# Kernel optimization log

Measured on AMD Instinct MI355X. Metric: run time of the kernel, lower is better.

Reference implementation:

```python
import jax, jax.numpy as jnp
import numpy as np

N, K, F, NRBF = 10000, 32, 128, 300
GAMMA = 10.0


def ssp(x):
    # shifted softplus: softplus(x) - log(2)
    return jax.nn.softplus(x) - jnp.log(2.0).astype(x.dtype)


def setup_inputs() -> dict:
    key = jax.random.key(0)
    ks = jax.random.split(key, 12)
    s = lambda fan_in: 1.0 / np.sqrt(fan_in)
    inp = {
        "xyz": jax.random.normal(ks[0], (N, 3), jnp.float32) * 5.0,
        "atomic": jax.random.normal(ks[1], (N, F), jnp.float32),
        "edge_mask": (jax.random.uniform(ks[2], (N, K)) < 0.9).astype(jnp.float32),
        "src": jax.random.randint(ks[3], (N, K), 0, N),
        # pre_conv Linear(F, F) with bias
        "W_pre": jax.random.uniform(ks[4], (F, F), jnp.float32, -s(F), s(F)),
        "b_pre": jax.random.uniform(ks[5], (F,), jnp.float32, -s(F), s(F)),
        # cfconv: Linear(300, F, bias=False), SSP, Linear(F, F, bias=False), SSP
        "W_cf1": jax.random.uniform(ks[6], (NRBF, F), jnp.float32, -s(NRBF), s(NRBF)),
        "W_cf2": jax.random.uniform(ks[7], (F, F), jnp.float32, -s(F), s(F)),
        # post_conv: Linear(F,F), SSP, Linear(F,F)
        "W_post1": jax.random.uniform(ks[8], (F, F), jnp.float32, -s(F), s(F)),
        "b_post1": jax.random.uniform(ks[9], (F,), jnp.float32, -s(F), s(F)),
        "W_post2": jax.random.uniform(ks[10], (F, F), jnp.float32, -s(F), s(F)),
        "b_post2": jax.random.uniform(ks[11], (F,), jnp.float32, -s(F), s(F)),
        "rbf_centers": jnp.linspace(0.1, 30.1, NRBF, dtype=jnp.float32),
    }
    return inp


def reference(xyz, atomic, edge_mask, src, W_pre, b_pre, W_cf1, W_cf2,
              W_post1, b_post1, W_post2, b_post2, rbf_centers):
    pre = atomic @ W_pre + b_pre                       # [N, F]
    nbr_xyz = xyz[src]                                 # gather: [N, K, 3]
    d_ij = jnp.linalg.norm(nbr_xyz - xyz[:, None, :], axis=2, keepdims=True)  # [N, K, 1]
    rbf = jnp.exp(-GAMMA * (d_ij - rbf_centers[None, None, :]) ** 2)          # [N, K, 300]
    filters = ssp(ssp(rbf @ W_cf1) @ W_cf2)            # [N, K, F]
    conv_out = jnp.sum(filters * pre[src] * edge_mask[:, :, None], axis=1)    # [N, F]
    post = ssp(conv_out @ W_post1 + b_post1) @ W_post2 + b_post2
    return atomic + post
```

## Files before the change

### kernel.cpp

```cpp
#include <hip/hip_runtime.h>

#define NATOMS 10000
#define KNB 32
#define FD 128
#define NRBF 300
#define STEPC (30.0f / 299.0f)
#define INVSTEP (299.0f / 30.0f)
#define TROWS 256

typedef short short8 __attribute__((ext_vector_type(8)));
typedef float f32x4 __attribute__((ext_vector_type(4)));
typedef unsigned int u32x4 __attribute__((ext_vector_type(4)));

__device__ __forceinline__ unsigned short f2bf_rne(float f) {
    unsigned int u = __float_as_uint(f);
    u = (u + 0x7fffu + ((u >> 16) & 1u)) >> 16;
    return (unsigned short)u;
}

__device__ __forceinline__ unsigned int pack_bf2(float hi, float lo) {
    return __builtin_amdgcn_perm(__float_as_uint(hi) + 0x8000u,
                                 __float_as_uint(lo) + 0x8000u, 0x07060302u);
}

__device__ __forceinline__ unsigned short f2bf_rhu(float f) {
    return (unsigned short)((__float_as_uint(f) + 0x8000u) >> 16);
}

__device__ __forceinline__ float ssp_fast(float x) {
    float t = __builtin_amdgcn_exp2f(x * 1.44269504f);
    float l = __builtin_amdgcn_logf(1.0f + t);
    return 0.69314718056f * (l - 1.0f);
}

__device__ __forceinline__ float ssp_poly(float x) {
    float u = x * x;
    float p = fmaf(u, 2.1356923e-6f, -2.6351976e-5f);
    p = fmaf(u, p, 3.2552083e-4f);
    p = fmaf(u, p, -5.2083333e-3f);
    p = fmaf(u, p, 0.125f);
    return fmaf(0.5f, x, u * p);
}

__device__ __forceinline__ void gload_lds16(const void* g, void* l) {
    __builtin_amdgcn_global_load_lds(
        (const __attribute__((address_space(1))) unsigned int*)g,
        (__attribute__((address_space(3))) unsigned int*)l, 16, 0, 0);
}

__device__ __forceinline__ short8 rbf_row8(float d, float cg) {
    float t = d - cg;
    t = fminf(3.5f, fmaxf(-3.5f, t));
    float r = __builtin_amdgcn_exp2f(-14.4269504f * t * t);
    float q = __builtin_amdgcn_exp2f((28.8539008f * STEPC) * t
                                     - (14.4269504f * STEPC * STEPC));
    const float QRATIO = 0.81763172f;
    u32x4 p;
#pragma unroll
    for (int jj = 0; jj < 4; ++jj) {
        float v0 = r; r *= q; q *= QRATIO;
        float v1 = r; r *= q; q *= QRATIO;
        p[jj] = pack_bf2(v1, v0);
    }
    return __builtin_bit_cast(short8, p);
}

__global__ __launch_bounds__(256) void prep_pack(
    const float* __restrict__ Wcf1, const float* __restrict__ Wpre,
    const float* __restrict__ Wcf2, const float* __restrict__ Wpost1,
    const float* __restrict__ Wpost2, unsigned short* __restrict__ w1p,
    unsigned short* __restrict__ w4p) {
    int idx = blockIdx.x * 256 + threadIdx.x;
    if (idx < 40960) {
        int j = idx & 7, c = (idx >> 3) & 127, g = (idx >> 10) & 3, kc = idx >> 12;
        int k = kc * 32 + g * 8 + j;
        float v = (k < NRBF) ? Wcf1[k * FD + c] : 0.f;
        w1p[idx] = f2bf_rne(v);
    } else if (idx < 40960 + 65536) {
        int t = idx - 40960;
        int sel = t >> 14;
        int t2 = t & 16383;
        int j = t2 & 7, c = (t2 >> 3) & 127, g = (t2 >> 10) & 3, kc = t2 >> 12;
        int k = kc * 32 + g * 8 + j;
        const float* W = (sel == 0) ? Wpre : (sel == 1) ? Wcf2 : (sel == 2) ? Wpost1 : Wpost2;
        w4p[t] = f2bf_rne(W[k * FD + c]);
    }
}

__global__ __launch_bounds__(256) void pre_and_table(
    const float* __restrict__ X, const unsigned short* __restrict__ Wp,
    const float* __restrict__ bias, unsigned int* __restrict__ preP,
    const unsigned short* __restrict__ w1p, const unsigned short* __restrict__ w2p,
    unsigned int* __restrict__ T) {
    __shared__ unsigned short A2[128][132];
    const int tid = threadIdx.x;
    const int w = tid >> 6, lane = tid & 63, g = lane >> 4, c16 = lane & 15;

    if (blockIdx.x < 157) {
        const int r0 = blockIdx.x * 64 + w * 16;
        f32x4 acc[8];
#pragma unroll
        for (int b = 0; b < 8; ++b) acc[b] = (f32x4){0.f, 0.f, 0.f, 0.f};
        int row = r0 + c16;
        if (row >= NATOMS) row = 0;
#pragma unroll
        for (int kc = 0; kc < 4; ++kc) {
            const float* p0 = X + (size_t)row * FD + kc * 32 + g * 8;
            float4 xa = *(const float4*)p0, xb = *(const float4*)(p0 + 4);
            u32x4 pa;
            pa[0] = pack_bf2(xa.y, xa.x); pa[1] = pack_bf2(xa.w, xa.z);
            pa[2] = pack_bf2(xb.y, xb.x); pa[3] = pack_bf2(xb.w, xb.z);
            short8 a0 = __builtin_bit_cast(short8, pa);
            const unsigned short* wb = Wp + (kc * 4 + g) * 1024 + c16 * 8;
#pragma unroll
            for (int nb = 0; nb < 8; ++nb) {
                short8 b = *(const short8*)(wb + nb * 128);
                acc[nb] = __builtin_amdgcn_mfma_f32_16x16x32_bf16(a0, b, acc[nb], 0, 0, 0);
            }
        }
        float bv[8];
#pragma unroll
        for (int nb = 0; nb < 8; ++nb) bv[nb] = bias[nb * 16 + c16];
#pragma unroll
        for (int q = 0; q < 4; ++q) {
            int orow = r0 + 4 * g + q;
            if (orow < NATOMS) {
#pragma unroll
                for (int p2 = 0; p2 < 4; ++p2) {
                    float v0 = acc[2 * p2][q] + bv[2 * p2];
                    float v1 = acc[2 * p2 + 1][q] + bv[2 * p2 + 1];
                    preP[orow * 64 + c16 * 4 + p2] = pack_bf2(v1, v0);
                }
            }
        }
        return;
    }

    const int rbase = (int)(blockIdx.x - 157) * 128 + w * 32;
    const float hstep = 0.125f;
    const float d0 = (float)(rbase + c16) * hstep;
    const float d1 = (float)(rbase + 16 + c16) * hstep;

    const float BAND = 1.05f;
    float lo = (float)rbase * hstep, hi = (float)(rbase + 31) * hstep;
    int L = max(0, (int)floorf(((lo - BAND - 0.1f) * INVSTEP - 31.f) * 0.03125f));
    int H = min(9, (int)floorf(((hi + BAND - 0.1f) * INVSTEP) * 0.03125f));

    f32x4 acc[2][8];
#pragma unroll
    for (int a = 0; a < 2; ++a)
#pragma unroll
        for (int b = 0; b < 8; ++b) acc[a][b] = (f32x4){0.f, 0.f, 0.f, 0.f};

    for (int kc = L; kc <= H; ++kc) {
        const unsigned short* wb = w1p + kc * 4096 + g * 1024 + c16 * 8;
        short8 bfr[8];
#pragma unroll
        for (int nb = 0; nb < 8; ++nb) bfr[nb] = *(const short8*)(wb + nb * 128);
        const float cg = 0.1f + (float)(kc * 32 + g * 8) * STEPC;
        short8 a0 = rbf_row8(d0, cg);
        short8 a1 = rbf_row8(d1, cg);
#pragma unroll
        for (int nb = 0; nb < 8; ++nb) {
            acc[0][nb] = __builtin_amdgcn_mfma_f32_16x16x32_bf16(a0, bfr[nb], acc[0][nb], 0, 0, 0);
            acc[1][nb] = __builtin_amdgcn_mfma_f32_16x16x32_bf16(a1, bfr[nb], acc[1][nb], 0, 0, 0);
        }
    }

#pragma unroll
    for (int mr = 0; mr < 2; ++mr)
#pragma unroll
        for (int nb = 0; nb < 8; ++nb)
#pragma unroll
            for (int q = 0; q < 4; ++q) {
                int row = w * 32 + mr * 16 + 4 * g + q;
                A2[row][nb * 16 + c16] = f2bf_rhu(ssp_poly(acc[mr][nb][q]));
            }

    f32x4 acc2[2][8];
#pragma unroll
    for (int a = 0; a < 2; ++a)
#pragma unroll
        for (int b = 0; b < 8; ++b) acc2[a][b] = (f32x4){0.f, 0.f, 0.f, 0.f};

#pragma unroll
    for (int kc = 0; kc < 4; ++kc) {
        short8 a0 = *(const short8*)&A2[w * 32 + c16][kc * 32 + g * 8];
        short8 a1 = *(const short8*)&A2[w * 32 + 16 + c16][kc * 32 + g * 8];
        const unsigned short* wb = w2p + (kc * 4 + g) * 1024 + c16 * 8;
#pragma unroll
        for (int nb = 0; nb < 8; ++nb) {
            short8 b = *(const short8*)(wb + nb * 128);
            acc2[0][nb] = __builtin_amdgcn_mfma_f32_16x16x32_bf16(a0, b, acc2[0][nb], 0, 0, 0);
            acc2[1][nb] = __builtin_amdgcn_mfma_f32_16x16x32_bf16(a1, b, acc2[1][nb], 0, 0, 0);
        }
    }

#pragma unroll
    for (int mr = 0; mr < 2; ++mr)
#pragma unroll
        for (int q = 0; q < 4; ++q) {
            int r = rbase + mr * 16 + 4 * g + q;
#pragma unroll
            for (int p2 = 0; p2 < 4; ++p2) {
                float F0 = ssp_poly(acc2[mr][2 * p2][q]);
                float F1 = ssp_poly(acc2[mr][2 * p2 + 1][q]);
                T[r * 64 + c16 * 4 + p2] =
                    ((unsigned int)f2bf_rne(F1) << 16) | f2bf_rne(F0);
            }
        }
}

__global__ __launch_bounds__(512, 4) void conv_post(
    const float* __restrict__ xyz, const int* __restrict__ src,
    const float* __restrict__ mask, const unsigned int* __restrict__ preP,
    const unsigned int* __restrict__ T, const unsigned short* __restrict__ w1,
    const float* __restrict__ b1, const unsigned short* __restrict__ w2,
    const float* __restrict__ b2, const float* __restrict__ resid,
    float* __restrict__ Y) {
    __shared__ unsigned int Tl[TROWS * 64];
    __shared__ unsigned short Aconv[16][132];

    const int tid = threadIdx.x;
    const int w = tid >> 6;
    const int lane = tid & 63;
    const int l5 = lane & 31;
    const int c16 = lane & 15;
    const int g = lane >> 4;

#pragma unroll
    for (int it = 0; it < 8; ++it) {
        const unsigned int* gp = T + w * 2048 + it * 256 + lane * 4;
        gload_lds16(gp, &Tl[w * 2048 + it * 256]);
    }

    const int iA = blockIdx.x * 16 + w;
    const int iB = iA + 8;

    int svA = src[iA * KNB + l5];
    int svB = src[iB * KNB + l5];
    float mvA = mask[iA * KNB + l5];
    float mvB = mask[iB * KNB + l5];
    float dxA = xyz[3 * svA]     - xyz[3 * iA];
    float dyA = xyz[3 * svA + 1] - xyz[3 * iA + 1];
    float dzA = xyz[3 * svA + 2] - xyz[3 * iA + 2];
    float dxB = xyz[3 * svB]     - xyz[3 * iB];
    float dyB = xyz[3 * svB + 1] - xyz[3 * iB + 1];
    float dzB = xyz[3 * svB + 2] - xyz[3 * iB + 2];
    float dA = sqrtf(dxA * dxA + dyA * dyA + dzA * dzA);
    float dB = sqrtf(dxB * dxB + dyB * dyB + dzB * dzB);
    dA = (mvA > 0.f) ? dA : 1e9f;
    dB = (mvB > 0.f) ? dB : 1e9f;
    float tA = fminf(dA * 8.0f, (float)(TROWS - 2) + 0.999f);
    float tB = fminf(dB * 8.0f, (float)(TROWS - 2) + 0.999f);
    float fiA = floorf(tA), fiB = floorf(tB);
    float frA = tA - fiA,  frB = tB - fiB;
    int iiA = (int)fiA, iiB = (int)fiB;

    __syncthreads();

    float a00 = 0.f, a01 = 0.f, a10 = 0.f, a11 = 0.f;
#pragma unroll
    for (int eb = 0; eb < KNB; eb += 8) {
        unsigned int tA0[8], tB0[8], tA1[8], tB1[8], q0[8], q1[8];
        float fr0[8], fr1[8];
#pragma unroll
        for (int j = 0; j < 8; ++j) {
            const int e = eb + j;
            int ie0 = __builtin_amdgcn_readlane(iiA, e);
            int se0 = __builtin_amdgcn_readlane(svA, e);
            fr0[j] = __uint_as_float((unsigned int)__builtin_amdgcn_readlane(
                         (int)__float_as_uint(frA), e));
            int ie1 = __builtin_amdgcn_readlane(iiB, e);
            int se1 = __builtin_amdgcn_readlane(svB, e);
            fr1[j] = __uint_as_float((unsigned int)__builtin_amdgcn_readlane(
                         (int)__float_as_uint(frB), e));
            q0[j] = preP[se0 * 64 + lane];
            q1[j] = preP[se1 * 64 + lane];
            tA0[j] = Tl[ie0 * 64 + lane];
            tB0[j] = Tl[ie0 * 64 + 64 + lane];
            tA1[j] = Tl[ie1 * 64 + lane];
            tB1[j] = Tl[ie1 * 64 + 64 + lane];
        }
#pragma unroll
        for (int j = 0; j < 8; ++j) {
            float A00 = __uint_as_float(tA0[j] << 16);
            float A01 = __uint_as_float(tA0[j] & 0xffff0000u);
            float B00 = __uint_as_float(tB0[j] << 16);
            float B01 = __uint_as_float(tB0[j] & 0xffff0000u);
            float f00 = fmaf(fr0[j], B00 - A00, A00);
            float f01 = fmaf(fr0[j], B01 - A01, A01);
            a00 = fmaf(f00, __uint_as_float(q0[j] << 16), a00);
            a01 = fmaf(f01, __uint_as_float(q0[j] & 0xffff0000u), a01);
            float A10 = __uint_as_float(tA1[j] << 16);
            float A11 = __uint_as_float(tA1[j] & 0xffff0000u);
            float B10 = __uint_as_float(tB1[j] << 16);
            float B11 = __uint_as_float(tB1[j] & 0xffff0000u);
            float f10 = fmaf(fr1[j], B10 - A10, A10);
            float f11 = fmaf(fr1[j], B11 - A11, A11);
            a10 = fmaf(f10, __uint_as_float(q1[j] << 16), a10);
            a11 = fmaf(f11, __uint_as_float(q1[j] & 0xffff0000u), a11);
        }
    }
    {
        int c0 = 32 * (lane & 3) + (lane >> 2);
        Aconv[w][c0]          = f2bf_rhu(a00);
        Aconv[w][c0 + 16]     = f2bf_rhu(a01);
        Aconv[w + 8][c0]      = f2bf_rhu(a10);
        Aconv[w + 8][c0 + 16] = f2bf_rhu(a11);
    }
    __syncthreads();

    unsigned short* Amid = (unsigned short*)Tl;
    const int r0 = blockIdx.x * 16;

    f32x4 acc = (f32x4){0.f, 0.f, 0.f, 0.f};
#pragma unroll
    for (int kc = 0; kc < 4; ++kc) {
        short8 a0 = *(const short8*)&Aconv[c16][kc * 32 + g * 8];
        const unsigned short* wb = w1 + (kc * 4 + g) * 1024;
        short8 b = *(const short8*)(wb + (w * 16 + c16) * 8);
        acc = __builtin_amdgcn_mfma_f32_16x16x32_bf16(a0, b, acc, 0, 0, 0);
    }
    {
        float bv = b1[w * 16 + c16];
#pragma unroll
        for (int q = 0; q < 4; ++q)
            Amid[(4 * g + q) * 132 + w * 16 + c16] =
                f2bf_rhu(ssp_fast(acc[q] + bv));
    }
    __syncthreads();

    f32x4 acc2 = (f32x4){0.f, 0.f, 0.f, 0.f};
#pragma unroll
    for (int kc = 0; kc < 4; ++kc) {
        short8 a0 = *(const short8*)&Amid[c16 * 132 + kc * 32 + g * 8];
        const unsigned short* wb = w2 + (kc * 4 + g) * 1024;
        short8 b = *(const short8*)(wb + (w * 16 + c16) * 8);
        acc2 = __builtin_amdgcn_mfma_f32_16x16x32_bf16(a0, b, acc2, 0, 0, 0);
    }
    {
        float bv2 = b2[w * 16 + c16];
#pragma unroll
        for (int q = 0; q < 4; ++q) {
            int o = (r0 + 4 * g + q) * FD + w * 16 + c16;
            Y[o] = acc2[q] + bv2 + resid[o];
        }
    }
}

extern "C" void kernel_launch(void* const* d_in, const int* in_sizes, int n_in,
                              void* d_out, int out_size, void* d_ws, size_t ws_size,
                              hipStream_t stream) {
    const float* xyz     = (const float*)d_in[0];
    const float* atomic  = (const float*)d_in[1];
    const float* mask    = (const float*)d_in[2];
    const int*   src     = (const int*)d_in[3];
    const float* W_pre   = (const float*)d_in[4];
    const float* b_pre   = (const float*)d_in[5];
    const float* W_cf1   = (const float*)d_in[6];
    const float* W_cf2   = (const float*)d_in[7];
    const float* W_post1 = (const float*)d_in[8];
    const float* b_post1 = (const float*)d_in[9];
    const float* W_post2 = (const float*)d_in[10];
    const float* b_post2 = (const float*)d_in[11];
    float* out = (float*)d_out;

    unsigned int*   preP = (unsigned int*)d_ws;
    unsigned int*   T    = (unsigned int*)((char*)d_ws + 2560000);
    unsigned short* w1p  = (unsigned short*)((char*)d_ws + 2625536);
    unsigned short* w4p  = w1p + 40960;
    unsigned short* wpre   = w4p;
    unsigned short* wcf2   = w4p + 16384;
    unsigned short* wpost1 = w4p + 32768;
    unsigned short* wpost2 = w4p + 49152;

    prep_pack<<<416, 256, 0, stream>>>(W_cf1, W_pre, W_cf2, W_post1, W_post2, w1p, w4p);
    pre_and_table<<<159, 256, 0, stream>>>(atomic, wpre, b_pre, preP, w1p, wcf2, T);
    conv_post<<<625, 512, 0, stream>>>(xyz, src, mask, preP, T,
                                       wpost1, b_post1, wpost2, b_post2, atomic, out);
}
```

Baseline: 39.91 us.

## Process 20 atoms per block and shrink distance table to 252 rows

The conv_post kernel now handles 20 atoms per block instead of 16, so 500 blocks run instead of 625. Warps 0-3 each take one extra atom, and the two post MLP matmuls run over 32 padded rows. The table is trimmed to 252 rows, which cuts the per-block LDS fill (63 chunks instead of 64) and shared memory use. The aim is to spread the fixed per-block table load across more atoms and cut the block count. In exchange, four warps do extra work that lengthens the critical path, distances are clamped to a slightly shorter range, and the padded rows add wasted MFMA work.

```diff
diff --git a/kernel.cpp b/kernel.cpp
--- a/kernel.cpp
+++ b/kernel.cpp
@@ -6,7 +6,7 @@
 #define NRBF 300
 #define STEPC (30.0f / 299.0f)
 #define INVSTEP (299.0f / 30.0f)
-#define TROWS 256
+#define TROWS 252
 
 typedef short short8 __attribute__((ext_vector_type(8)));
 typedef float f32x4 __attribute__((ext_vector_type(4)));
@@ -201,12 +201,14 @@
 #pragma unroll
         for (int q = 0; q < 4; ++q) {
             int r = rbase + mr * 16 + 4 * g + q;
-#pragma unroll
-            for (int p2 = 0; p2 < 4; ++p2) {
-                float F0 = ssp_poly(acc2[mr][2 * p2][q]);
-                float F1 = ssp_poly(acc2[mr][2 * p2 + 1][q]);
-                T[r * 64 + c16 * 4 + p2] =
-                    ((unsigned int)f2bf_rne(F1) << 16) | f2bf_rne(F0);
+            if (r < TROWS) {
+#pragma unroll
+                for (int p2 = 0; p2 < 4; ++p2) {
+                    float F0 = ssp_poly(acc2[mr][2 * p2][q]);
+                    float F1 = ssp_poly(acc2[mr][2 * p2 + 1][q]);
+                    T[r * 64 + c16 * 4 + p2] =
+                        ((unsigned int)f2bf_rne(F1) << 16) | f2bf_rne(F0);
+                }
             }
         }
 }
@@ -219,7 +221,7 @@
     const float* __restrict__ b2, const float* __restrict__ resid,
     float* __restrict__ Y) {
     __shared__ unsigned int Tl[TROWS * 64];
-    __shared__ unsigned short Aconv[16][132];
+    __shared__ unsigned short Aconv[32][132];
 
     const int tid = threadIdx.x;
     const int w = tid >> 6;
@@ -230,11 +232,14 @@
 
 #pragma unroll
     for (int it = 0; it < 8; ++it) {
-        const unsigned int* gp = T + w * 2048 + it * 256 + lane * 4;
-        gload_lds16(gp, &Tl[w * 2048 + it * 256]);
-    }
-
-    const int iA = blockIdx.x * 16 + w;
+        if ((w << 3) + it < 63) {
+            const unsigned int* gp = T + w * 2048 + it * 256 + lane * 4;
+            gload_lds16(gp, &Tl[w * 2048 + it * 256]);
+        }
+    }
+
+    const int base = blockIdx.x * 20;
+    const int iA = base + w;
     const int iB = iA + 8;
 
     int svA = src[iA * KNB + l5];
@@ -257,6 +262,22 @@
     float frA = tA - fiA,  frB = tB - fiB;
     int iiA = (int)fiA, iiB = (int)fiB;
 
+    int svC = 0; float frC = 0.f; int iiC = 0;
+    if (w < 4) {
+        int iC = base + 16 + w;
+        svC = src[iC * KNB + l5];
+        float mvC = mask[iC * KNB + l5];
+        float dxC = xyz[3 * svC]     - xyz[3 * iC];
+        float dyC = xyz[3 * svC + 1] - xyz[3 * iC + 1];
+        float dzC = xyz[3 * svC + 2] - xyz[3 * iC + 2];
+        float dC = sqrtf(dxC * dxC + dyC * dyC + dzC * dzC);
+        dC = (mvC > 0.f) ? dC : 1e9f;
+        float tC = fminf(dC * 8.0f, (float)(TROWS - 2) + 0.999f);
+        float fiC = floorf(tC);
+        frC = tC - fiC;
+        iiC = (int)fiC;
+    }
+
     __syncthreads();
 
     float a00 = 0.f, a01 = 0.f, a10 = 0.f, a11 = 0.f;
@@ -309,43 +330,94 @@
         Aconv[w + 8][c0]      = f2bf_rhu(a10);
         Aconv[w + 8][c0 + 16] = f2bf_rhu(a11);
     }
+
+    if (w < 4) {
+        float c00 = 0.f, c01 = 0.f;
+#pragma unroll
+        for (int eb = 0; eb < KNB; eb += 8) {
+            unsigned int tAc[8], tBc[8], qc[8];
+            float frc[8];
+#pragma unroll
+            for (int j = 0; j < 8; ++j) {
+                const int e = eb + j;
+                int ie = __builtin_amdgcn_readlane(iiC, e);
+                int se = __builtin_amdgcn_readlane(svC, e);
+                frc[j] = __uint_as_float((unsigned int)__builtin_amdgcn_readlane(
+                             (int)__float_as_uint(frC), e));
+                qc[j] = preP[se * 64 + lane];
+                tAc[j] = Tl[ie * 64 + lane];
+                tBc[j] = Tl[ie * 64 + 64 + lane];
+            }
+#pragma unroll
+            for (int j = 0; j < 8; ++j) {
+                float Ac0 = __uint_as_float(tAc[j] << 16);
+                float Ac1 = __uint_as_float(tAc[j] & 0xffff0000u);
+                float Bc0 = __uint_as_float(tBc[j] << 16);
+                float Bc1 = __uint_as_float(tBc[j] & 0xffff0000u);
+                float fc0 = fmaf(frc[j], Bc0 - Ac0, Ac0);
+                float fc1 = fmaf(frc[j], Bc1 - Ac1, Ac1);
+                c00 = fmaf(fc0, __uint_as_float(qc[j] << 16), c00);
+                c01 = fmaf(fc1, __uint_as_float(qc[j] & 0xffff0000u), c01);
+            }
+        }
+        int c0 = 32 * (lane & 3) + (lane >> 2);
+        Aconv[16 + w][c0]      = f2bf_rhu(c00);
+        Aconv[16 + w][c0 + 16] = f2bf_rhu(c01);
+    }
+
+    for (int idx = tid; idx < 12 * 132; idx += 512)
+        (&Aconv[20][0])[idx] = 0;
+
     __syncthreads();
 
     unsigned short* Amid = (unsigned short*)Tl;
-    const int r0 = blockIdx.x * 16;
-
-    f32x4 acc = (f32x4){0.f, 0.f, 0.f, 0.f};
+    f32x4 acc[2];
+    acc[0] = (f32x4){0.f, 0.f, 0.f, 0.f};
+    acc[1] = (f32x4){0.f, 0.f, 0.f, 0.f};
 #pragma unroll
     for (int kc = 0; kc < 4; ++kc) {
         short8 a0 = *(const short8*)&Aconv[c16][kc * 32 + g * 8];
+        short8 a1 = *(const short8*)&Aconv[16 + c16][kc * 32 + g * 8];
         const unsigned short* wb = w1 + (kc * 4 + g) * 1024;
         short8 b = *(const short8*)(wb + (w * 16 + c16) * 8);
-        acc = __builtin_amdgcn_mfma_f32_16x16x32_bf16(a0, b, acc, 0, 0, 0);
+        acc[0] = __builtin_amdgcn_mfma_f32_16x16x32_bf16(a0, b, acc[0], 0, 0, 0);
+        acc[1] = __builtin_amdgcn_mfma_f32_16x16x32_bf16(a1, b, acc[1], 0, 0, 0);
     }
     {
         float bv = b1[w * 16 + c16];
 #pragma unroll
-        for (int q = 0; q < 4; ++q)
-            Amid[(4 * g + q) * 132 + w * 16 + c16] =
-                f2bf_rhu(ssp_fast(acc[q] + bv));
+        for (int mr = 0; mr < 2; ++mr)
+#pragma unroll
+            for (int q = 0; q < 4; ++q)
+                Amid[(mr * 16 + 4 * g + q) * 132 + w * 16 + c16] =
+                    f2bf_rhu(ssp_fast(acc[mr][q] + bv));
     }
     __syncthreads();
 
-    f32x4 acc2 = (f32x4){0.f, 0.f, 0.f, 0.f};
+    f32x4 acc2[2];
+    acc2[0] = (f32x4){0.f, 0.f, 0.f, 0.f};
+    acc2[1] = (f32x4){0.f, 0.f, 0.f, 0.f};
 #pragma unroll
     for (int kc = 0; kc < 4; ++kc) {
         short8 a0 = *(const short8*)&Amid[c16 * 132 + kc * 32 + g * 8];
+        short8 a1 = *(const short8*)&Amid[(16 + c16) * 132 + kc * 32 + g * 8];
         const unsigned short* wb = w2 + (kc * 4 + g) * 1024;
         short8 b = *(const short8*)(wb + (w * 16 + c16) * 8);
-        acc2 = __builtin_amdgcn_mfma_f32_16x16x32_bf16(a0, b, acc2, 0, 0, 0);
+        acc2[0] = __builtin_amdgcn_mfma_f32_16x16x32_bf16(a0, b, acc2[0], 0, 0, 0);
+        acc2[1] = __builtin_amdgcn_mfma_f32_16x16x32_bf16(a1, b, acc2[1], 0, 0, 0);
     }
     {
         float bv2 = b2[w * 16 + c16];
 #pragma unroll
-        for (int q = 0; q < 4; ++q) {
-            int o = (r0 + 4 * g + q) * FD + w * 16 + c16;
-            Y[o] = acc2[q] + bv2 + resid[o];
-        }
+        for (int mr = 0; mr < 2; ++mr)
+#pragma unroll
+            for (int q = 0; q < 4; ++q) {
+                int rl = mr * 16 + 4 * g + q;
+                if (rl < 20) {
+                    int o = (base + rl) * FD + w * 16 + c16;
+                    Y[o] = acc2[mr][q] + bv2 + resid[o];
+                }
+            }
     }
 }
 
@@ -377,6 +449,6 @@
 
     prep_pack<<<416, 256, 0, stream>>>(W_cf1, W_pre, W_cf2, W_post1, W_post2, w1p, w4p);
     pre_and_table<<<159, 256, 0, stream>>>(atomic, wpre, b_pre, preP, w1p, wcf2, T);
-    conv_post<<<625, 512, 0, stream>>>(xyz, src, mask, preP, T,
+    conv_post<<<500, 512, 0, stream>>>(xyz, src, mask, preP, T,
                                        wpost1, b_post1, wpost2, b_post2, atomic, out);
 }
```

Measured after the change: 41.27 us. 3.4% more time.
